# Kernel tuning notes

Hardware: AMD Instinct MI355X
Metric: run time of the kernel (lower is better)

The kernel has to match this reference:

```python
import jax, jax.numpy as jnp
import numpy as np

# --- GridEncoder config (matches torch-ngp defaults) ---
D = 3                 # input_dim
L = 16                # num_levels
C = 2                 # level_dim
H = 16                # base_resolution
PLS = 2.0             # per_level_scale
LOG2_HASHMAP = 19
MAX_PARAMS = 2 ** LOG2_HASHMAP
PRIMES = (1, 2654435761, 805459861)  # fast_hash primes for D=3
ALIGN_CORNERS = False


def _level_meta():
    """Replicates the offsets computation in GridEncoder.__init__ and the
    kernel's per-level resolution / hash-vs-dense decision."""
    metas = []
    off = 0
    for l in range(L):
        res = int(np.ceil(H * PLS ** l))            # kernel: ceil(exp2(l*S)*H - 1) + 1 == H*2^l here
        full = (res if ALIGN_CORNERS else res + 1) ** D
        params = min(MAX_PARAMS, full)
        params = int(np.ceil(params / 8) * 8)       # pad to multiple of 8
        hashed = full > params                      # kernel: stride > hashmap_size after index loop
        metas.append((off, params, res, hashed))
        off += params
    return metas, off

METAS, TOTAL_PARAMS = _level_meta()


def setup_inputs() -> dict:
    key = jax.random.key(0)
    k1, k2 = jax.random.split(key)
    B = 1048576
    inputs = jax.random.uniform(k1, (B, D), dtype=jnp.float32, minval=-1.0, maxval=1.0)
    # reset_parameters(): uniform(-1e-4, 1e-4)
    embeddings = jax.random.uniform(k2, (TOTAL_PARAMS, C), dtype=jnp.float32,
                                    minval=-1e-4, maxval=1e-4)
    return {"inputs": inputs, "embeddings": embeddings}


def _grid_encode(x, embeddings):
    """x: [B, D] in [0, 1]. Returns [B, L*C]."""
    corner_bits = jnp.array([[(c >> d) & 1 for d in range(D)] for c in range(2 ** D)],
                            dtype=jnp.uint32)                       # [8, D]
    primes = jnp.array(PRIMES, dtype=jnp.uint32)
    outs = []
    for l, (off, size, res, hashed) in enumerate(METAS):
        scale = float(np.exp2(l) * H - 1.0)                          # exp2(l*S)*H - 1, S = log2(2) = 1
        pos = x * scale + (0.0 if ALIGN_CORNERS else 0.5)            # [B, D]
        pg_f = jnp.floor(pos)
        frac = pos - pg_f                                            # [B, D] linear interp weights
        pg = pg_f.astype(jnp.uint32)                                 # [B, D]
        corners = pg[None, :, :] + corner_bits[:, None, :]           # [8, B, D]
        # N-linear interpolation weights: prod over dims of frac / (1-frac)
        w = jnp.prod(jnp.where(corner_bits[:, None, :] == 1,
                               frac[None, :, :], 1.0 - frac[None, :, :]), axis=-1)  # [8, B]
        if hashed:
            # fast_hash: xor of pos_grid[d] * primes[d] in wrapping uint32
            idx = corners[..., 0] * primes[0]
            for d in range(1, D):
                idx = idx ^ (corners[..., d] * primes[d])
        else:
            base = res if ALIGN_CORNERS else res + 1
            stride = jnp.array([base ** d for d in range(D)], dtype=jnp.uint32)
            idx = (corners * stride).sum(axis=-1).astype(jnp.uint32)
        idx = (idx % jnp.uint32(size)) + jnp.uint32(off)             # [8, B]
        emb = embeddings[idx]                                        # [8, B, C] gather
        outs.append(jnp.einsum('kb,kbc->bc', w, emb))                # [B, C]
    return jnp.concatenate(outs, axis=-1)                            # [B, L*C], level-major


def reference(inputs, embeddings):
    bound = 1.0
    x = (inputs + bound) / (2.0 * bound)   # map to [0, 1]
    return _grid_encode(x, embeddings)
```

## Files before the change

### kernel.cpp

```cpp
#include <hip/hip_runtime.h>
#include <cstdint>


namespace {

using f32x2 = __attribute__((ext_vector_type(2))) float;
using f32x4 = __attribute__((ext_vector_type(4))) float;

__device__ __forceinline__ void level_setup_g(
    float x, float y, float z, uint32_t l,
    uint32_t g[8], float f[6]) {
  uint32_t res = 16u << l;
  float scale = (float)res - 1.0f;
  float px = x * scale + 0.5f;
  float py = y * scale + 0.5f;
  float pz = z * scale + 0.5f;
  float gx = floorf(px), gy = floorf(py), gz = floorf(pz);
  float rx = px - gx, ry = py - gy, rz = pz - gz;
  uint32_t ix = (uint32_t)gx, iy = (uint32_t)gy, iz = (uint32_t)gz;

  if (l >= 3u) {
    uint32_t off = l * 524288u - 1257368u;
    const uint32_t P2 = 2654435761u, P3 = 805459861u;
    uint32_t hy0 = iy * P2, hy1 = hy0 + P2;
    uint32_t hz0 = iz * P3, hz1 = hz0 + P3;
    uint32_t hb[4] = {hy0 ^ hz0, hy1 ^ hz0, hy0 ^ hz1, hy1 ^ hz1};
    uint32_t ix1 = ix + 1u;
#pragma unroll
    for (int j = 0; j < 4; ++j) {
      g[2 * j]     = ((ix  ^ hb[j]) & 0x7FFFFu) + off;
      g[2 * j + 1] = ((ix1 ^ hb[j]) & 0x7FFFFu) + off;
    }
  } else {
    uint32_t off = (l == 0u) ? 0u : ((l == 1u) ? 4920u : 40864u);
    uint32_t base = res + 1u;
    uint32_t bb = base * base;
    uint32_t dy0 = iy * base, dy1 = dy0 + base;
    uint32_t dz0 = iz * bb,   dz1 = dz0 + bb;
#pragma unroll
    for (int c = 0; c < 8; ++c) {
      g[c] = ix + (uint32_t)(c & 1) +
             ((c & 2) ? dy1 : dy0) + ((c & 4) ? dz1 : dz0) + off;
    }
  }
  f[0] = 1.0f - rx; f[1] = rx;
  f[2] = 1.0f - ry; f[3] = ry;
  f[4] = 1.0f - rz; f[5] = rz;
}

__device__ __forceinline__ f32x2 interp8(const f32x2 e[8], const float f[6]) {
  float o0 = 0.0f, o1 = 0.0f;
#pragma unroll
  for (int c = 0; c < 8; ++c) {
    float w = f[c & 1] * f[2 + ((c >> 1) & 1)] * f[4 + ((c >> 2) & 1)];
    o0 = fmaf(w, e[c].x, o0);
    o1 = fmaf(w, e[c].y, o1);
  }
  f32x2 r; r.x = o0; r.y = o1;
  return r;
}

__global__ __launch_bounds__(256) void prep_xyz_kernel(
    const float* __restrict__ in,
    float* __restrict__ X, float* __restrict__ Y, float* __restrict__ Z,
    uint32_t B) {
  uint32_t t = blockIdx.x * 256u + threadIdx.x;
  uint32_t nquad = B >> 2;
  if (t >= nquad) return;
  const f32x4* in4 = reinterpret_cast<const f32x4*>(in);
  f32x4 q0 = __builtin_nontemporal_load(&in4[t * 3 + 0]);
  f32x4 q1 = __builtin_nontemporal_load(&in4[t * 3 + 1]);
  f32x4 q2 = __builtin_nontemporal_load(&in4[t * 3 + 2]);
  f32x4 xv = {q0.x, q0.w, q1.z, q2.y};
  f32x4 yv = {q0.y, q1.x, q1.w, q2.z};
  f32x4 zv = {q0.z, q1.y, q2.x, q2.w};
  xv = (xv + 1.0f) * 0.5f;
  yv = (yv + 1.0f) * 0.5f;
  zv = (zv + 1.0f) * 0.5f;
  reinterpret_cast<f32x4*>(X)[t] = xv;
  reinterpret_cast<f32x4*>(Y)[t] = yv;
  reinterpret_cast<f32x4*>(Z)[t] = zv;
}

template <bool XYZ>
__global__ __launch_bounds__(256, 6) void gather_lm_kernel(
    const float* __restrict__ in,
    const float* __restrict__ X, const float* __restrict__ Y,
    const float* __restrict__ Z,
    const f32x2* __restrict__ emb,
    f32x2* __restrict__ ws,
    uint32_t B) {
  uint32_t l = blockIdx.y;
  uint32_t p0 = blockIdx.x * 512u + threadIdx.x;
  uint32_t p1 = p0 + 256u;
  bool vA = p0 < B, vB = p1 < B;
  if (!vA) return;
  uint32_t p1c = vB ? p1 : p0;

  float xA, yA, zA, xB, yB, zB;
  if (XYZ) {
    xA = X[p0]; yA = Y[p0]; zA = Z[p0];
    xB = X[p1c]; yB = Y[p1c]; zB = Z[p1c];
  } else {
    xA = (__builtin_nontemporal_load(&in[p0 * 3 + 0]) + 1.0f) * 0.5f;
    yA = (__builtin_nontemporal_load(&in[p0 * 3 + 1]) + 1.0f) * 0.5f;
    zA = (__builtin_nontemporal_load(&in[p0 * 3 + 2]) + 1.0f) * 0.5f;
    xB = (__builtin_nontemporal_load(&in[p1c * 3 + 0]) + 1.0f) * 0.5f;
    yB = (__builtin_nontemporal_load(&in[p1c * 3 + 1]) + 1.0f) * 0.5f;
    zB = (__builtin_nontemporal_load(&in[p1c * 3 + 2]) + 1.0f) * 0.5f;
  }

  uint32_t gA[8]; float fA[6];
  level_setup_g(xA, yA, zA, l, gA, fA);
  f32x2 eA[8];
#pragma unroll
  for (int c = 0; c < 8; ++c) eA[c] = emb[gA[c]];

  uint32_t gB[8]; float fB[6];
  level_setup_g(xB, yB, zB, l, gB, fB);
  f32x2 eB[8];
#pragma unroll
  for (int c = 0; c < 8; ++c) eB[c] = emb[gB[c]];

  f32x2 rA = interp8(eA, fA);
  __builtin_nontemporal_store(rA, &ws[(size_t)l * B + p0]);
  if (vB) {
    f32x2 rB = interp8(eB, fB);
    __builtin_nontemporal_store(rB, &ws[(size_t)l * B + p1]);
  }
}

__global__ __launch_bounds__(256) void transpose_kernel(
    const f32x2* __restrict__ ws,
    f32x4* __restrict__ out,
    uint32_t B) {
  uint32_t n = (B >> 1) * 8u;
  uint32_t t = blockIdx.x * 256u + threadIdx.x;
  if (t >= n) return;
  uint32_t j = t & 7u;
  uint32_t q0 = (t >> 3) * 2u;
  const f32x4* ws4 = reinterpret_cast<const f32x4*>(ws);
  f32x4 va = ws4[((size_t)(2u * j)      * B + q0) >> 1];
  f32x4 vb = ws4[((size_t)(2u * j + 1u) * B + q0) >> 1];
  f32x4 v0 = {va.x, va.y, vb.x, vb.y};
  f32x4 v1 = {va.z, va.w, vb.z, vb.w};
  __builtin_nontemporal_store(v0, &out[(size_t)q0 * 8u + j]);
  __builtin_nontemporal_store(v1, &out[(size_t)(q0 + 1u) * 8u + j]);
}

__global__ __launch_bounds__(256) void grid_encode_fallback(
    const float* __restrict__ in, const f32x2* __restrict__ emb,
    f32x2* __restrict__ out, uint32_t B) {
  uint32_t p = blockIdx.x * 256u + threadIdx.x;
  if (p >= B) return;
  float x = (in[p * 3 + 0] + 1.0f) * 0.5f;
  float y = (in[p * 3 + 1] + 1.0f) * 0.5f;
  float z = (in[p * 3 + 2] + 1.0f) * 0.5f;
#pragma unroll 1
  for (uint32_t l = 0; l < 16u; ++l) {
    uint32_t g[8]; float f[6];
    level_setup_g(x, y, z, l, g, f);
    f32x2 e[8];
#pragma unroll
    for (int c = 0; c < 8; ++c) e[c] = emb[g[c]];
    out[(size_t)p * 16u + l] = interp8(e, f);
  }
}

}

extern "C" void kernel_launch(void* const* d_in, const int* in_sizes, int n_in,
                              void* d_out, int out_size, void* d_ws, size_t ws_size,
                              hipStream_t stream) {
  (void)n_in; (void)out_size;
  const float* in = (const float*)d_in[0];
  const f32x2* emb = (const f32x2*)d_in[1];
  uint32_t B = (uint32_t)(in_sizes[0] / 3);

  size_t ws_lm   = (size_t)16 * B * sizeof(f32x2);
  size_t ws_full = ws_lm + (size_t)3 * B * sizeof(float);

  if ((B % 4u) == 0u && ws_size >= ws_lm) {
    f32x2* ws = (f32x2*)d_ws;
    uint32_t gblocks = (B + 511u) / 512u;
    bool use_xyz = ws_size >= ws_full;
    if (use_xyz) {
      float* X = (float*)((char*)d_ws + ws_lm);
      float* Y = X + B;
      float* Z = Y + B;
      uint32_t pblocks = ((B >> 2) + 255u) / 256u;
      hipLaunchKernelGGL(prep_xyz_kernel, dim3(pblocks), dim3(256), 0, stream,
                         in, X, Y, Z, B);
      hipLaunchKernelGGL((gather_lm_kernel<true>), dim3(gblocks, 16), dim3(256),
                         0, stream, in, X, Y, Z, emb, ws, B);
    } else {
      hipLaunchKernelGGL((gather_lm_kernel<false>), dim3(gblocks, 16), dim3(256),
                         0, stream, in, nullptr, nullptr, nullptr, emb, ws, B);
    }
    uint32_t tblocks = ((B >> 1) * 8u + 255u) / 256u;
    hipLaunchKernelGGL(transpose_kernel, dim3(tblocks), dim3(256), 0, stream,
                       ws, (f32x4*)d_out, B);
  } else {
    uint32_t pblocks = (B + 255u) / 256u;
    hipLaunchKernelGGL(grid_encode_fallback, dim3(pblocks), dim3(256), 0,
                       stream, in, emb, (f32x2*)d_out, B);
  }
}
```

Baseline: 599.1 us.

## Write gather results directly to output and drop transpose kernel

The gather kernel now writes each level's 8-byte result straight into the point-major output (stride of 16 levels) instead of into a level-major workspace. This removes the separate transpose pass and the round trip through a 128 MB workspace. The cost is that each wavefront's stores are now strided 128 bytes apart, so writes are scattered 8-byte partial-line stores. Occupancy hint drops from 6 to 5 and the XYZ loads become nontemporal.

```diff
diff --git a/kernel.cpp b/kernel.cpp
--- a/kernel.cpp
+++ b/kernel.cpp
@@ -83,12 +83,12 @@
 }
 
 template <bool XYZ>
-__global__ __launch_bounds__(256, 6) void gather_lm_kernel(
+__global__ __launch_bounds__(256, 5) void gather_direct_kernel(
     const float* __restrict__ in,
     const float* __restrict__ X, const float* __restrict__ Y,
     const float* __restrict__ Z,
     const f32x2* __restrict__ emb,
-    f32x2* __restrict__ ws,
+    f32x2* __restrict__ out,
     uint32_t B) {
   uint32_t l = blockIdx.y;
   uint32_t p0 = blockIdx.x * 512u + threadIdx.x;
@@ -99,8 +99,12 @@
 
   float xA, yA, zA, xB, yB, zB;
   if (XYZ) {
-    xA = X[p0]; yA = Y[p0]; zA = Z[p0];
-    xB = X[p1c]; yB = Y[p1c]; zB = Z[p1c];
+    xA = __builtin_nontemporal_load(&X[p0]);
+    yA = __builtin_nontemporal_load(&Y[p0]);
+    zA = __builtin_nontemporal_load(&Z[p0]);
+    xB = __builtin_nontemporal_load(&X[p1c]);
+    yB = __builtin_nontemporal_load(&Y[p1c]);
+    zB = __builtin_nontemporal_load(&Z[p1c]);
   } else {
     xA = (__builtin_nontemporal_load(&in[p0 * 3 + 0]) + 1.0f) * 0.5f;
     yA = (__builtin_nontemporal_load(&in[p0 * 3 + 1]) + 1.0f) * 0.5f;
@@ -123,29 +127,11 @@
   for (int c = 0; c < 8; ++c) eB[c] = emb[gB[c]];
 
   f32x2 rA = interp8(eA, fA);
-  __builtin_nontemporal_store(rA, &ws[(size_t)l * B + p0]);
+  __builtin_nontemporal_store(rA, &out[(size_t)p0 * 16u + l]);
   if (vB) {
     f32x2 rB = interp8(eB, fB);
-    __builtin_nontemporal_store(rB, &ws[(size_t)l * B + p1]);
+    __builtin_nontemporal_store(rB, &out[(size_t)p1 * 16u + l]);
   }
-}
-
-__global__ __launch_bounds__(256) void transpose_kernel(
-    const f32x2* __restrict__ ws,
-    f32x4* __restrict__ out,
-    uint32_t B) {
-  uint32_t n = (B >> 1) * 8u;
-  uint32_t t = blockIdx.x * 256u + threadIdx.x;
-  if (t >= n) return;
-  uint32_t j = t & 7u;
-  uint32_t q0 = (t >> 3) * 2u;
-  const f32x4* ws4 = reinterpret_cast<const f32x4*>(ws);
-  f32x4 va = ws4[((size_t)(2u * j)      * B + q0) >> 1];
-  f32x4 vb = ws4[((size_t)(2u * j + 1u) * B + q0) >> 1];
-  f32x4 v0 = {va.x, va.y, vb.x, vb.y};
-  f32x4 v1 = {va.z, va.w, vb.z, vb.w};
-  __builtin_nontemporal_store(v0, &out[(size_t)q0 * 8u + j]);
-  __builtin_nontemporal_store(v1, &out[(size_t)(q0 + 1u) * 8u + j]);
 }
 
 __global__ __launch_bounds__(256) void grid_encode_fallback(
@@ -175,34 +161,31 @@
   (void)n_in; (void)out_size;
   const float* in = (const float*)d_in[0];
   const f32x2* emb = (const f32x2*)d_in[1];
+  f32x2* out = (f32x2*)d_out;
   uint32_t B = (uint32_t)(in_sizes[0] / 3);
 
-  size_t ws_lm   = (size_t)16 * B * sizeof(f32x2);
-  size_t ws_full = ws_lm + (size_t)3 * B * sizeof(float);
+  size_t xyz_bytes = (size_t)3 * B * sizeof(float);
 
-  if ((B % 4u) == 0u && ws_size >= ws_lm) {
-    f32x2* ws = (f32x2*)d_ws;
+  if ((B % 4u) == 0u) {
     uint32_t gblocks = (B + 511u) / 512u;
-    bool use_xyz = ws_size >= ws_full;
+    bool use_xyz = ws_size >= xyz_bytes;
     if (use_xyz) {
-      float* X = (float*)((char*)d_ws + ws_lm);
+      float* X = (float*)d_ws;
       float* Y = X + B;
       float* Z = Y + B;
       uint32_t pblocks = ((B >> 2) + 255u) / 256u;
       hipLaunchKernelGGL(prep_xyz_kernel, dim3(pblocks), dim3(256), 0, stream,
                          in, X, Y, Z, B);
-      hipLaunchKernelGGL((gather_lm_kernel<true>), dim3(gblocks, 16), dim3(256),
-                         0, stream, in, X, Y, Z, emb, ws, B);
+      hipLaunchKernelGGL((gather_direct_kernel<true>), dim3(gblocks, 16),
+                         dim3(256), 0, stream, in, X, Y, Z, emb, out, B);
     } else {
-      hipLaunchKernelGGL((gather_lm_kernel<false>), dim3(gblocks, 16), dim3(256),
-                         0, stream, in, nullptr, nullptr, nullptr, emb, ws, B);
+      hipLaunchKernelGGL((gather_direct_kernel<false>), dim3(gblocks, 16),
+                         dim3(256), 0, stream, in, nullptr, nullptr, nullptr,
+                         emb, out, B);
     }
-    uint32_t tblocks = ((B >> 1) * 8u + 255u) / 256u;
-    hipLaunchKernelGGL(transpose_kernel, dim3(tblocks), dim3(256), 0, stream,
-                       ws, (f32x4*)d_out, B);
   } else {
     uint32_t pblocks = (B + 255u) / 256u;
     hipLaunchKernelGGL(grid_encode_fallback, dim3(pblocks), dim3(256), 0,
-                       stream, in, emb, (f32x2*)d_out, B);
+                       stream, in, emb, out, B);
   }
 }
```

Result: slower. 899.5 us (+50.1%).

## Stage transpose through LDS tiles, tweak gather occupancy and use nontemporal XYZ loads

Applied to the files above, without the earlier changes.

The level-major to point-major transpose now loads a 16x256-point tile into padded shared memory and writes fully contiguous output rows, replacing the strided per-thread reads and writes. The gather kernel's minimum-blocks hint drops from 6 to 5, which may give it more registers per thread, and the X/Y/Z loads become nontemporal. The fast path now requires B divisible by 256 and uses regular stores instead of nontemporal ones for the output.

```diff
diff --git a/kernel.cpp b/kernel.cpp
--- a/kernel.cpp
+++ b/kernel.cpp
@@ -83,7 +83,7 @@
 }
 
 template <bool XYZ>
-__global__ __launch_bounds__(256, 6) void gather_lm_kernel(
+__global__ __launch_bounds__(256, 5) void gather_lm_kernel(
     const float* __restrict__ in,
     const float* __restrict__ X, const float* __restrict__ Y,
     const float* __restrict__ Z,
@@ -99,8 +99,12 @@
 
   float xA, yA, zA, xB, yB, zB;
   if (XYZ) {
-    xA = X[p0]; yA = Y[p0]; zA = Z[p0];
-    xB = X[p1c]; yB = Y[p1c]; zB = Z[p1c];
+    xA = __builtin_nontemporal_load(&X[p0]);
+    yA = __builtin_nontemporal_load(&Y[p0]);
+    zA = __builtin_nontemporal_load(&Z[p0]);
+    xB = __builtin_nontemporal_load(&X[p1c]);
+    yB = __builtin_nontemporal_load(&Y[p1c]);
+    zB = __builtin_nontemporal_load(&Z[p1c]);
   } else {
     xA = (__builtin_nontemporal_load(&in[p0 * 3 + 0]) + 1.0f) * 0.5f;
     yA = (__builtin_nontemporal_load(&in[p0 * 3 + 1]) + 1.0f) * 0.5f;
@@ -130,22 +134,35 @@
   }
 }
 
-__global__ __launch_bounds__(256) void transpose_kernel(
+__global__ __launch_bounds__(256) void transpose_lds_kernel(
     const f32x2* __restrict__ ws,
     f32x4* __restrict__ out,
     uint32_t B) {
-  uint32_t n = (B >> 1) * 8u;
-  uint32_t t = blockIdx.x * 256u + threadIdx.x;
-  if (t >= n) return;
-  uint32_t j = t & 7u;
-  uint32_t q0 = (t >> 3) * 2u;
+  __shared__ f32x4 lds4[16][129];
+  uint32_t tid = threadIdx.x;
+  uint32_t cb = blockIdx.x * 256u;
+
   const f32x4* ws4 = reinterpret_cast<const f32x4*>(ws);
-  f32x4 va = ws4[((size_t)(2u * j)      * B + q0) >> 1];
-  f32x4 vb = ws4[((size_t)(2u * j + 1u) * B + q0) >> 1];
-  f32x4 v0 = {va.x, va.y, vb.x, vb.y};
-  f32x4 v1 = {va.z, va.w, vb.z, vb.w};
-  __builtin_nontemporal_store(v0, &out[(size_t)q0 * 8u + j]);
-  __builtin_nontemporal_store(v1, &out[(size_t)(q0 + 1u) * 8u + j]);
+#pragma unroll
+  for (uint32_t m = 0; m < 8u; ++m) {
+    uint32_t lin = m * 256u + tid;
+    uint32_t row = lin >> 7;
+    uint32_t pos = lin & 127u;
+    lds4[row][pos] = ws4[(((size_t)row * B + cb) >> 1) + pos];
+  }
+  __syncthreads();
+
+  const f32x2* lds2 = reinterpret_cast<const f32x2*>(lds4);
+#pragma unroll
+  for (uint32_t m = 0; m < 8u; ++m) {
+    uint32_t lin = m * 256u + tid;
+    uint32_t q = lin >> 3;
+    uint32_t j = lin & 7u;
+    f32x2 a = lds2[(2u * j)      * 258u + q];
+    f32x2 b = lds2[(2u * j + 1u) * 258u + q];
+    f32x4 v = {a.x, a.y, b.x, b.y};
+    out[(size_t)(cb + q) * 8u + j] = v;
+  }
 }
 
 __global__ __launch_bounds__(256) void grid_encode_fallback(
@@ -180,7 +197,7 @@
   size_t ws_lm   = (size_t)16 * B * sizeof(f32x2);
   size_t ws_full = ws_lm + (size_t)3 * B * sizeof(float);
 
-  if ((B % 4u) == 0u && ws_size >= ws_lm) {
+  if ((B % 256u) == 0u && ws_size >= ws_lm) {
     f32x2* ws = (f32x2*)d_ws;
     uint32_t gblocks = (B + 511u) / 512u;
     bool use_xyz = ws_size >= ws_full;
@@ -197,9 +214,9 @@
       hipLaunchKernelGGL((gather_lm_kernel<false>), dim3(gblocks, 16), dim3(256),
                          0, stream, in, nullptr, nullptr, nullptr, emb, ws, B);
     }
-    uint32_t tblocks = ((B >> 1) * 8u + 255u) / 256u;
-    hipLaunchKernelGGL(transpose_kernel, dim3(tblocks), dim3(256), 0, stream,
-                       ws, (f32x4*)d_out, B);
+    uint32_t tblocks = B / 256u;
+    hipLaunchKernelGGL(transpose_lds_kernel, dim3(tblocks), dim3(256), 0,
+                       stream, ws, (f32x4*)d_out, B);
   } else {
     uint32_t pblocks = (B + 255u) / 256u;
     hipLaunchKernelGGL(grid_encode_fallback, dim3(pblocks), dim3(256), 0,
```

After: 619.9 us. +3.5%, slower.
